# Kernel tuning notes

Measured on AMD Instinct MI355X. Metric: run time of the kernel, lower is better.

## Reference

```python
import jax, jax.numpy as jnp
import numpy as np

B, H, S, D = 2, 8, 2048, 64  # batch, heads, seq_len, depth (= F_hidden)
LEAKY_SLOPE = 0.2            # tf.nn.leaky_relu default alpha
EPS_ADJ = 1e-9


def setup_inputs() -> dict:
    key = jax.random.key(0)
    ks = jax.random.split(key, 8)
    scale = 1.0 / np.sqrt(D)  # glorot-ish for square [D,D] fan
    return {
        "Hin": jax.random.normal(ks[0], (B, H, S, D), jnp.float32),
        "Hk": jax.random.normal(ks[1], (B, H, S, D), jnp.float32),
        "Hv": jax.random.normal(ks[2], (B, H, S, D), jnp.float32),
        "A": jax.random.normal(ks[3], (B, H, D, D), jnp.float32),
        "mask": jnp.zeros((B, 1, 1, S), jnp.float32),
        "W": jax.random.normal(ks[4], (H, D, D), jnp.float32) * scale,
        "b": jnp.zeros((H, D, D), jnp.float32),
        "a_vec": jax.random.normal(ks[5], (H, D, D), jnp.float32) * scale,
        "ba": jnp.zeros((H, D, D), jnp.float32),
        "pw": jax.random.normal(ks[6], (H, D, D), jnp.float32) * scale,
    }


def reference(Hin, Hk, Hv, A, mask, W, b, a_vec, ba, pw):
    # AW = relu(W @ A + b) + eps          [B,H,D,D]
    AW = jax.nn.relu(jnp.einsum("hfd,bhde->bhfe", W, A) + b[None]) + EPS_ADJ
    # learned power transform on metric tensor
    Ap = AW ** pw[None]                   # [B,H,D,D]
    # energy curvature tensor: a @ Ap + ba
    avAp = jnp.einsum("hfd,bhde->bhfe", a_vec, Ap) + ba[None]  # [B,H,D,D]
    # attention scores: (Hin @ avAp) @ Hk^T / sqrt(dk)
    WHiWHj = jnp.einsum("bhsf,bhfe->bhse", Hin, avAp)          # [B,H,S,D]
    Ep = jnp.einsum("bhse,bhte->bhst", WHiWHj, Hk)             # [B,H,S,S]
    Ep = Ep / jnp.sqrt(jnp.float32(D))
    Ep = jax.nn.leaky_relu(Ep, LEAKY_SLOPE)
    E = jax.nn.softmax(Ep + mask * (-1e9), axis=-1)            # [B,H,S,S]
    # value matmul + output activation (relu); att_head=1 so concat == single head
    H_next = jax.nn.relu(jnp.einsum("bhst,bhtd->bhsd", E, Hv))  # [B,H,S,D]
    return H_next
```

## Files before the change

### kernel.cpp

```cpp
#include <hip/hip_runtime.h>
#include <cmath>

#define B_ 2
#define H_ 8
#define S_ 2048
#define D_ 64
#define TS 64
#define NT (S_ / TS)
#define LDST 68

typedef __attribute__((ext_vector_type(8))) _Float16 f16x8;
typedef __attribute__((ext_vector_type(4))) float f32x4;

__global__ __launch_bounds__(256) void prep_avAp(
    const float* __restrict__ A, const float* __restrict__ W,
    const float* __restrict__ bb, const float* __restrict__ av,
    const float* __restrict__ ba, const float* __restrict__ pw,
    float* __restrict__ avAp)
{
    __shared__ float s0[TS * LDST];
    __shared__ float s1[TS * LDST];
    const int tid = threadIdx.x;
    const int ty = tid >> 4, tx = tid & 15;
    const int bh = blockIdx.x;
    const int h = bh & (H_ - 1);

    const float4* W4 = (const float4*)(W + h * D_ * D_);
    const float4* A4 = (const float4*)(A + bh * D_ * D_);
#pragma unroll
    for (int it = 0; it < 4; ++it) {
        int idx = tid + it * 256;
        int r = idx >> 4, c = idx & 15;
        *(float4*)&s0[r * LDST + c * 4] = W4[idx];
        *(float4*)&s1[r * LDST + c * 4] = A4[idx];
    }
    __syncthreads();

    float acc[4][4] = {};
    for (int d = 0; d < D_; ++d) {
        float4 a4 = *(const float4*)&s1[d * LDST + tx * 4];
#pragma unroll
        for (int i = 0; i < 4; ++i) {
            float w = s0[(ty * 4 + i) * LDST + d];
            acc[i][0] += w * a4.x; acc[i][1] += w * a4.y;
            acc[i][2] += w * a4.z; acc[i][3] += w * a4.w;
        }
    }
    __syncthreads();

#pragma unroll
    for (int i = 0; i < 4; ++i) {
        int f = ty * 4 + i;
        float4 b4 = *(const float4*)&bb[(h * D_ + f) * D_ + tx * 4];
        float4 p4 = *(const float4*)&pw[(h * D_ + f) * D_ + tx * 4];
        float vb[4] = {b4.x, b4.y, b4.z, b4.w};
        float vp[4] = {p4.x, p4.y, p4.z, p4.w};
#pragma unroll
        for (int j = 0; j < 4; ++j) {
            float aw = fmaxf(acc[i][j] + vb[j], 0.f) + 1e-9f;
            s0[f * LDST + tx * 4 + j] = exp2f(vp[j] * __log2f(aw));
        }
    }
    const float4* av4 = (const float4*)(av + h * D_ * D_);
#pragma unroll
    for (int it = 0; it < 4; ++it) {
        int idx = tid + it * 256;
        int r = idx >> 4, c = idx & 15;
        *(float4*)&s1[r * LDST + c * 4] = av4[idx];
    }
    __syncthreads();

    float acc2[4][4] = {};
    for (int d = 0; d < D_; ++d) {
        float4 a4 = *(const float4*)&s0[d * LDST + tx * 4];
#pragma unroll
        for (int i = 0; i < 4; ++i) {
            float w = s1[(ty * 4 + i) * LDST + d];
            acc2[i][0] += w * a4.x; acc2[i][1] += w * a4.y;
            acc2[i][2] += w * a4.z; acc2[i][3] += w * a4.w;
        }
    }
#pragma unroll
    for (int i = 0; i < 4; ++i) {
        int f = ty * 4 + i;
        float4 ba4 = *(const float4*)&ba[(h * D_ + f) * D_ + tx * 4];
        float4 o = make_float4(acc2[i][0] + ba4.x, acc2[i][1] + ba4.y,
                               acc2[i][2] + ba4.z, acc2[i][3] + ba4.w);
        *(float4*)&avAp[bh * D_ * D_ + f * D_ + tx * 4] = o;
    }
}

#define KH_S 0
#define KL_S 8192
#define VT_S 16384
#define P_S  24576
#define QP_S 34816
#define AVP_S 0
#define HIN_S 17408
#define SMEM_SZ 52224

__global__ __launch_bounds__(256) void flash6(
    const float* __restrict__ Hin, const float* __restrict__ Hk,
    const float* __restrict__ Hv, const float* __restrict__ maskg,
    const float* __restrict__ avAp, float* __restrict__ out)
{
    __shared__ __align__(16) char smem[SMEM_SZ];
    float* AVP = (float*)(smem + AVP_S);
    float* HIN = (float*)(smem + HIN_S);
    float* QP  = (float*)(smem + QP_S);

    const int tid = threadIdx.x;
    const int wave = tid >> 6, lane = tid & 63;
    const int l15 = lane & 15, lg = lane >> 4;
    const int qt = blockIdx.x, bh = blockIdx.y;
    const int b = bh >> 3;
    const size_t base = (size_t)bh * S_ * D_;
    const int q0 = qt * TS;
    const float* mrow = maskg + b * S_;

    {
        const float4* a4 = (const float4*)(avAp + bh * D_ * D_);
        const float4* h4 = (const float4*)(Hin + base + (size_t)q0 * D_);
#pragma unroll
        for (int i = 0; i < 4; ++i) {
            int f = tid + i * 256;
            int r = f >> 4, c = (f & 15) * 4;
            *(float4*)&AVP[r * LDST + c] = a4[f];
            *(float4*)&HIN[r * LDST + c] = h4[f];
        }
    }
    __syncthreads();
    {
        const int tx = tid & 15, ty = tid >> 4;
        float acc[4][4] = {};
        for (int d = 0; d < D_; ++d) {
            float4 av = *(const float4*)&AVP[d * LDST + tx * 4];
#pragma unroll
            for (int rr = 0; rr < 4; ++rr) {
                float h = HIN[(ty * 4 + rr) * LDST + d];
                acc[rr][0] += h * av.x; acc[rr][1] += h * av.y;
                acc[rr][2] += h * av.z; acc[rr][3] += h * av.w;
            }
        }
#pragma unroll
        for (int rr = 0; rr < 4; ++rr)
            *(float4*)&QP[(ty * 4 + rr) * LDST + tx * 4] =
                make_float4(acc[rr][0], acc[rr][1], acc[rr][2], acc[rr][3]);
    }
    __syncthreads();

    f16x8 qAh[2], qAl[2];
#pragma unroll
    for (int kc = 0; kc < 2; ++kc) {
        int row = wave * 16 + l15;
        int k0 = kc * 32 + lg * 8;
        float4 v0 = *(const float4*)&QP[row * LDST + k0];
        float4 v1 = *(const float4*)&QP[row * LDST + k0 + 4];
        float xs[8] = {v0.x, v0.y, v0.z, v0.w, v1.x, v1.y, v1.z, v1.w};
#pragma unroll
        for (int j = 0; j < 8; ++j) {
            float x = xs[j] * 0.125f;
            _Float16 hh = (_Float16)x;
            qAh[kc][j] = hh;
            qAl[kc][j] = (_Float16)(x - (float)hh);
        }
    }

    float4 kreg[2][2], vreg[2][2];
    auto stage_load = [&](int kt) {
        const float* Kg = Hk + base + (size_t)kt * TS * D_;
        const float* Vg = Hv + base + (size_t)kt * TS * D_;
#pragma unroll
        for (int i = 0; i < 2; ++i) {
            int c = tid + i * 256;
            kreg[i][0] = *(const float4*)(Kg + c * 8);
            kreg[i][1] = *(const float4*)(Kg + c * 8 + 4);
            vreg[i][0] = *(const float4*)(Vg + c * 8);
            vreg[i][1] = *(const float4*)(Vg + c * 8 + 4);
        }
    };
    auto stage_write = [&]() {
#pragma unroll
        for (int i = 0; i < 2; ++i) {
            int c = tid + i * 256;
            int r = c >> 3, c8 = c & 7;
            float xs[8] = {kreg[i][0].x, kreg[i][0].y, kreg[i][0].z, kreg[i][0].w,
                           kreg[i][1].x, kreg[i][1].y, kreg[i][1].z, kreg[i][1].w};
            f16x8 h, l;
#pragma unroll
            for (int e = 0; e < 8; ++e) {
                _Float16 hh = (_Float16)xs[e];
                h[e] = hh; l[e] = (_Float16)(xs[e] - (float)hh);
            }
            int byte = (r * 128 + c8 * 16) ^ ((r & 7) << 4);
            *(f16x8*)(smem + KH_S + byte) = h;
            *(f16x8*)(smem + KL_S + byte) = l;
            float vs[8] = {vreg[i][0].x, vreg[i][0].y, vreg[i][0].z, vreg[i][0].w,
                           vreg[i][1].x, vreg[i][1].y, vreg[i][1].z, vreg[i][1].w};
#pragma unroll
            for (int e = 0; e < 8; ++e) {
                int vr = c8 * 8 + e;
                int vb = (vr * 128 + r * 2) ^
                         ((((vr & 7) ^ ((vr >> 3) & 7)) << 4));
                *(_Float16*)(smem + VT_S + vb) = (_Float16)vs[e];
            }
        }
    };

    stage_load(0);
    stage_write();
    __syncthreads();

    float mrun[4], lrun[4];
    f32x4 o[4];
#pragma unroll
    for (int i = 0; i < 4; ++i) {
        mrun[i] = -INFINITY; lrun[i] = 0.f;
        o[i] = (f32x4){0.f, 0.f, 0.f, 0.f};
    }

    for (int kt = 0; kt < NT; ++kt) {
        if (kt + 1 < NT) stage_load(kt + 1);

        float mk[4];
#pragma unroll
        for (int ns = 0; ns < 4; ++ns)
            mk[ns] = -1e9f * mrow[kt * TS + ns * 16 + l15];

        f32x4 s[4];
#pragma unroll
        for (int ns = 0; ns < 4; ++ns) s[ns] = (f32x4){0.f, 0.f, 0.f, 0.f};
        __builtin_amdgcn_s_setprio(1);
#pragma unroll
        for (int ns = 0; ns < 4; ++ns)
#pragma unroll
            for (int kc = 0; kc < 2; ++kc) {
                int row = ns * 16 + l15;
                int byte = (row * 128 + kc * 64 + lg * 16) ^ ((row & 7) << 4);
                f16x8 kh = *(const f16x8*)(smem + KH_S + byte);
                f16x8 kl = *(const f16x8*)(smem + KL_S + byte);
                s[ns] = __builtin_amdgcn_mfma_f32_16x16x32_f16(qAh[kc], kh, s[ns], 0, 0, 0);
                s[ns] = __builtin_amdgcn_mfma_f32_16x16x32_f16(qAl[kc], kh, s[ns], 0, 0, 0);
                s[ns] = __builtin_amdgcn_mfma_f32_16x16x32_f16(qAh[kc], kl, s[ns], 0, 0, 0);
            }
        __builtin_amdgcn_s_setprio(0);

        float scs[4];
#pragma unroll
        for (int r = 0; r < 4; ++r) {
            float v[4];
#pragma unroll
            for (int ns = 0; ns < 4; ++ns) {
                float x = s[ns][r];
                x = (x > 0.f) ? x : 0.2f * x;
                v[ns] = x + mk[ns];
            }
            float m0 = fmaxf(fmaxf(v[0], v[1]), fmaxf(v[2], v[3]));
#pragma unroll
            for (int off = 1; off < 16; off <<= 1)
                m0 = fmaxf(m0, __shfl_xor(m0, off, 64));
            float mnew = fmaxf(mrun[r], m0);
            float sc = __expf(mrun[r] - mnew);
            mrun[r] = mnew;
            float rs = 0.f;
            float p[4];
#pragma unroll
            for (int ns = 0; ns < 4; ++ns) { p[ns] = __expf(v[ns] - mnew); rs += p[ns]; }
#pragma unroll
            for (int off = 1; off < 16; off <<= 1)
                rs += __shfl_xor(rs, off, 64);
            lrun[r] = lrun[r] * sc + rs;
            scs[r] = sc;
            int prow = lg * 4 + r;
#pragma unroll
            for (int ns = 0; ns < 4; ++ns) {
                int pb = (prow * 128 + (ns * 16 + l15) * 2) ^ ((prow & 7) << 4);
                *(_Float16*)(smem + P_S + wave * 2048 + pb) = (_Float16)p[ns];
            }
        }
#pragma unroll
        for (int ns = 0; ns < 4; ++ns)
#pragma unroll
            for (int r = 0; r < 4; ++r) o[ns][r] *= scs[r];

        __syncthreads();

        __builtin_amdgcn_s_setprio(1);
#pragma unroll
        for (int kc = 0; kc < 2; ++kc) {
            int pb = (l15 * 128 + kc * 64 + lg * 16) ^ ((l15 & 7) << 4);
            f16x8 pf = *(const f16x8*)(smem + P_S + wave * 2048 + pb);
#pragma unroll
            for (int ns = 0; ns < 4; ++ns) {
                int vrow = ns * 16 + l15;
                int vb = (vrow * 128 + kc * 64 + lg * 16) ^
                         ((((vrow & 7) ^ ((vrow >> 3) & 7)) << 4));
                f16x8 vf = *(const f16x8*)(smem + VT_S + vb);
                o[ns] = __builtin_amdgcn_mfma_f32_16x16x32_f16(pf, vf, o[ns], 0, 0, 0);
            }
        }
        __builtin_amdgcn_s_setprio(0);

        __syncthreads();

        if (kt + 1 < NT) stage_write();

        __syncthreads();
    }

#pragma unroll
    for (int r = 0; r < 4; ++r) {
        float inv = 1.f / lrun[r];
        int row = q0 + wave * 16 + lg * 4 + r;
#pragma unroll
        for (int ns = 0; ns < 4; ++ns)
            out[base + (size_t)row * D_ + ns * 16 + l15] =
                fmaxf(o[ns][r] * inv, 0.f);
    }
}

extern "C" void kernel_launch(void* const* d_in, const int* in_sizes, int n_in,
                              void* d_out, int out_size, void* d_ws, size_t ws_size,
                              hipStream_t stream) {
    const float* Hin  = (const float*)d_in[0];
    const float* Hk   = (const float*)d_in[1];
    const float* Hv   = (const float*)d_in[2];
    const float* A    = (const float*)d_in[3];
    const float* mask = (const float*)d_in[4];
    const float* W    = (const float*)d_in[5];
    const float* bb   = (const float*)d_in[6];
    const float* av   = (const float*)d_in[7];
    const float* ba   = (const float*)d_in[8];
    const float* pw   = (const float*)d_in[9];
    float* out = (float*)d_out;
    float* ws  = (float*)d_ws;

    prep_avAp<<<B_ * H_, 256, 0, stream>>>(A, W, bb, av, ba, pw, ws);
    flash6<<<dim3(NT, B_ * H_), 256, 0, stream>>>(Hin, Hk, Hv, mask, ws, out);
}
```

Before: 183.6 us.

## Transpose score MFMA so P stays in registers, drop LDS round-trip

Swaps the MFMA operand order so each lane holds one query row's scores across columns. Row max and sum then need only two cross-lane shuffles, and one running max/sum serves the whole row. The P tile is packed to half2 and rearranged into the PV A-operand with lane shuffles instead of being written to and read from LDS, which also removes one __syncthreads. The mask is read with float4 loads and the output with float4 stores. The cost is extra ds_bpermute shuffles and selects per key tile.

```diff
diff --git a/kernel.cpp b/kernel.cpp
--- a/kernel.cpp
+++ b/kernel.cpp
@@ -1,4 +1,5 @@
 #include <hip/hip_runtime.h>
+#include <hip/hip_fp16.h>
 #include <cmath>
 
 #define B_ 2
@@ -93,13 +94,12 @@
 #define KH_S 0
 #define KL_S 8192
 #define VT_S 16384
-#define P_S  24576
 #define QP_S 34816
 #define AVP_S 0
 #define HIN_S 17408
 #define SMEM_SZ 52224
 
-__global__ __launch_bounds__(256) void flash6(
+__global__ __launch_bounds__(256) void flash7(
     const float* __restrict__ Hin, const float* __restrict__ Hk,
     const float* __restrict__ Hv, const float* __restrict__ maskg,
     const float* __restrict__ avAp, float* __restrict__ out)
@@ -211,21 +211,22 @@
     stage_write();
     __syncthreads();
 
-    float mrun[4], lrun[4];
+    float mrun = -INFINITY, lrun = 0.f;
     f32x4 o[4];
 #pragma unroll
-    for (int i = 0; i < 4; ++i) {
-        mrun[i] = -INFINITY; lrun[i] = 0.f;
-        o[i] = (f32x4){0.f, 0.f, 0.f, 0.f};
-    }
+    for (int i = 0; i < 4; ++i) o[i] = (f32x4){0.f, 0.f, 0.f, 0.f};
+
+    const int srcA = l15 + (lg & 1) * 32;
+    const int srcB = srcA + 16;
+    const int ns_sel = lg >> 1;
 
     for (int kt = 0; kt < NT; ++kt) {
         if (kt + 1 < NT) stage_load(kt + 1);
 
-        float mk[4];
+        float4 mk4[4];
 #pragma unroll
         for (int ns = 0; ns < 4; ++ns)
-            mk[ns] = -1e9f * mrow[kt * TS + ns * 16 + l15];
+            mk4[ns] = *(const float4*)&mrow[kt * TS + ns * 16 + lg * 4];
 
         f32x4 s[4];
 #pragma unroll
@@ -239,64 +240,80 @@
                 int byte = (row * 128 + kc * 64 + lg * 16) ^ ((row & 7) << 4);
                 f16x8 kh = *(const f16x8*)(smem + KH_S + byte);
                 f16x8 kl = *(const f16x8*)(smem + KL_S + byte);
-                s[ns] = __builtin_amdgcn_mfma_f32_16x16x32_f16(qAh[kc], kh, s[ns], 0, 0, 0);
-                s[ns] = __builtin_amdgcn_mfma_f32_16x16x32_f16(qAl[kc], kh, s[ns], 0, 0, 0);
-                s[ns] = __builtin_amdgcn_mfma_f32_16x16x32_f16(qAh[kc], kl, s[ns], 0, 0, 0);
+                s[ns] = __builtin_amdgcn_mfma_f32_16x16x32_f16(kh, qAh[kc], s[ns], 0, 0, 0);
+                s[ns] = __builtin_amdgcn_mfma_f32_16x16x32_f16(kl, qAh[kc], s[ns], 0, 0, 0);
+                s[ns] = __builtin_amdgcn_mfma_f32_16x16x32_f16(kh, qAl[kc], s[ns], 0, 0, 0);
             }
         __builtin_amdgcn_s_setprio(0);
 
-        float scs[4];
-#pragma unroll
-        for (int r = 0; r < 4; ++r) {
-            float v[4];
-#pragma unroll
-            for (int ns = 0; ns < 4; ++ns) {
+        float xmax = -INFINITY;
+#pragma unroll
+        for (int ns = 0; ns < 4; ++ns) {
+            float m[4] = {mk4[ns].x, mk4[ns].y, mk4[ns].z, mk4[ns].w};
+#pragma unroll
+            for (int r = 0; r < 4; ++r) {
                 float x = s[ns][r];
-                x = (x > 0.f) ? x : 0.2f * x;
-                v[ns] = x + mk[ns];
-            }
-            float m0 = fmaxf(fmaxf(v[0], v[1]), fmaxf(v[2], v[3]));
-#pragma unroll
-            for (int off = 1; off < 16; off <<= 1)
-                m0 = fmaxf(m0, __shfl_xor(m0, off, 64));
-            float mnew = fmaxf(mrun[r], m0);
-            float sc = __expf(mrun[r] - mnew);
-            mrun[r] = mnew;
-            float rs = 0.f;
-            float p[4];
-#pragma unroll
-            for (int ns = 0; ns < 4; ++ns) { p[ns] = __expf(v[ns] - mnew); rs += p[ns]; }
-#pragma unroll
-            for (int off = 1; off < 16; off <<= 1)
-                rs += __shfl_xor(rs, off, 64);
-            lrun[r] = lrun[r] * sc + rs;
-            scs[r] = sc;
-            int prow = lg * 4 + r;
-#pragma unroll
-            for (int ns = 0; ns < 4; ++ns) {
-                int pb = (prow * 128 + (ns * 16 + l15) * 2) ^ ((prow & 7) << 4);
-                *(_Float16*)(smem + P_S + wave * 2048 + pb) = (_Float16)p[ns];
-            }
-        }
+                x = fmaxf(x, 0.2f * x);
+                x = fmaf(m[r], -1e9f, x);
+                s[ns][r] = x;
+                xmax = fmaxf(xmax, x);
+            }
+        }
+        xmax = fmaxf(xmax, __shfl_xor(xmax, 16, 64));
+        xmax = fmaxf(xmax, __shfl_xor(xmax, 32, 64));
+        float mnew = fmaxf(mrun, xmax);
+        float sc = __expf(mrun - mnew);
+        mrun = mnew;
+        float rs = 0.f;
 #pragma unroll
         for (int ns = 0; ns < 4; ++ns)
 #pragma unroll
-            for (int r = 0; r < 4; ++r) o[ns][r] *= scs[r];
-
-        __syncthreads();
+            for (int r = 0; r < 4; ++r) {
+                float p = __expf(s[ns][r] - mnew);
+                s[ns][r] = p;
+                rs += p;
+            }
+        rs += __shfl_xor(rs, 16, 64);
+        rs += __shfl_xor(rs, 32, 64);
+        lrun = lrun * sc + rs;
+#pragma unroll
+        for (int ns = 0; ns < 4; ++ns)
+#pragma unroll
+            for (int r = 0; r < 4; ++r) o[ns][r] *= sc;
+
+        unsigned pk[4][2];
+#pragma unroll
+        for (int ns = 0; ns < 4; ++ns) {
+            __half2 h01 = __floats2half2_rn(s[ns][0], s[ns][1]);
+            __half2 h23 = __floats2half2_rn(s[ns][2], s[ns][3]);
+            pk[ns][0] = *(unsigned*)&h01;
+            pk[ns][1] = *(unsigned*)&h23;
+        }
 
         __builtin_amdgcn_s_setprio(1);
 #pragma unroll
         for (int kc = 0; kc < 2; ++kc) {
-            int pb = (l15 * 128 + kc * 64 + lg * 16) ^ ((l15 & 7) << 4);
-            f16x8 pf = *(const f16x8*)(smem + P_S + wave * 2048 + pb);
+            unsigned a0 = __shfl((int)pk[kc * 2][0], srcA, 64);
+            unsigned a1 = __shfl((int)pk[kc * 2][1], srcA, 64);
+            unsigned b0 = __shfl((int)pk[kc * 2 + 1][0], srcA, 64);
+            unsigned b1 = __shfl((int)pk[kc * 2 + 1][1], srcA, 64);
+            unsigned c0 = __shfl((int)pk[kc * 2][0], srcB, 64);
+            unsigned c1 = __shfl((int)pk[kc * 2][1], srcB, 64);
+            unsigned d0 = __shfl((int)pk[kc * 2 + 1][0], srcB, 64);
+            unsigned d1 = __shfl((int)pk[kc * 2 + 1][1], srcB, 64);
+            unsigned w[4];
+            w[0] = ns_sel ? b0 : a0;
+            w[1] = ns_sel ? b1 : a1;
+            w[2] = ns_sel ? d0 : c0;
+            w[3] = ns_sel ? d1 : c1;
+            f16x8 pf = *(f16x8*)w;
 #pragma unroll
             for (int ns = 0; ns < 4; ++ns) {
                 int vrow = ns * 16 + l15;
                 int vb = (vrow * 128 + kc * 64 + lg * 16) ^
                          ((((vrow & 7) ^ ((vrow >> 3) & 7)) << 4));
                 f16x8 vf = *(const f16x8*)(smem + VT_S + vb);
-                o[ns] = __builtin_amdgcn_mfma_f32_16x16x32_f16(pf, vf, o[ns], 0, 0, 0);
+                o[ns] = __builtin_amdgcn_mfma_f32_16x16x32_f16(vf, pf, o[ns], 0, 0, 0);
             }
         }
         __builtin_amdgcn_s_setprio(0);
@@ -308,14 +325,17 @@
         __syncthreads();
     }
 
-#pragma unroll
-    for (int r = 0; r < 4; ++r) {
-        float inv = 1.f / lrun[r];
-        int row = q0 + wave * 16 + lg * 4 + r;
-#pragma unroll
-        for (int ns = 0; ns < 4; ++ns)
-            out[base + (size_t)row * D_ + ns * 16 + l15] =
-                fmaxf(o[ns][r] * inv, 0.f);
+    {
+        float inv = 1.f / lrun;
+        int row = q0 + wave * 16 + l15;
+#pragma unroll
+        for (int ns = 0; ns < 4; ++ns) {
+            float4 v = make_float4(fmaxf(o[ns][0] * inv, 0.f),
+                                   fmaxf(o[ns][1] * inv, 0.f),
+                                   fmaxf(o[ns][2] * inv, 0.f),
+                                   fmaxf(o[ns][3] * inv, 0.f));
+            *(float4*)&out[base + (size_t)row * D_ + ns * 16 + lg * 4] = v;
+        }
     }
 }
 
@@ -336,5 +356,5 @@
     float* ws  = (float*)d_ws;
 
     prep_avAp<<<B_ * H_, 256, 0, stream>>>(A, W, bb, av, ba, pw, ws);
-    flash6<<<dim3(NT, B_ * H_), 256, 0, stream>>>(Hin, Hk, Hv, mask, ws, out);
+    flash7<<<dim3(NT, B_ * H_), 256, 0, stream>>>(Hin, Hk, Hv, mask, ws, out);
 }
```

After: 169.0 us. -7.9%, faster.
